# Performance work log

Measured on AMD Instinct MI355X. Metric: run time of the kernel, lower is better.

Reference implementation:

```python
import jax, jax.numpy as jnp
import numpy as np

N, E, F, S, R, H = 10000, 160000, 128, 10, 8, 64
SH_OFF = [0, 1, 4, 9]
SH_DIM = [1, 3, 5, 7]
AVG_NUM_NEIGHBORS = 16.0


def setup_inputs() -> dict:
    key = jax.random.key(0)
    ks = jax.random.split(key, 16)
    species = jax.random.randint(ks[0], (N,), 0, S)
    node_attrs = jax.nn.one_hot(species, S, dtype=jnp.float32)
    node_feats = jax.random.normal(ks[1], (N, F), dtype=jnp.float32)
    edge_attrs = jax.random.normal(ks[2], (E, 16), dtype=jnp.float32)
    edge_feats = jax.random.normal(ks[3], (E, R), dtype=jnp.float32)
    edge_index = jax.random.randint(ks[4], (2, E), 0, N)
    # learned parameters
    W_skip_node = jax.random.normal(ks[5], (F, S, F), dtype=jnp.float32)
    W_up = jax.random.normal(ks[6], (F, F), dtype=jnp.float32)
    mlp_w1 = jax.random.normal(ks[7], (R, H), dtype=jnp.float32)
    mlp_w2 = jax.random.normal(ks[8], (H, H), dtype=jnp.float32)
    mlp_w3 = jax.random.normal(ks[9], (H, H), dtype=jnp.float32)
    mlp_w4 = jax.random.normal(ks[10], (H, 4 * F), dtype=jnp.float32)  # conv_tp.weight_numel = 512
    W_lin = jax.random.normal(ks[11], (4, F, F), dtype=jnp.float32)
    W_skip_msg = jax.random.normal(ks[12], (4, F, S, F), dtype=jnp.float32)
    W_out = jax.random.normal(ks[13], (F, F), dtype=jnp.float32)
    return dict(node_attrs=node_attrs, node_feats=node_feats, edge_attrs=edge_attrs,
                edge_feats=edge_feats, edge_index=edge_index, species=species,
                W_skip_node=W_skip_node, W_up=W_up, mlp_w1=mlp_w1, mlp_w2=mlp_w2,
                mlp_w3=mlp_w3, mlp_w4=mlp_w4, W_lin=W_lin, W_skip_msg=W_skip_msg,
                W_out=W_out)


def reference(node_attrs, node_feats, edge_attrs, edge_feats, edge_index, species,
              W_skip_node, W_up, mlp_w1, mlp_w2, mlp_w3, mlp_w4,
              W_lin, W_skip_msg, W_out):
    sender, receiver = edge_index[0], edge_index[1]
    num_nodes = node_feats.shape[0]
    num_edges = edge_attrs.shape[0]

    # skip_tp_node: FullyConnectedTensorProduct(128x0e, 10x0e -> 128x0e), fan_in = 128*10
    skip = jnp.einsum('nu,nv,uvw->nw', node_feats, node_attrs, W_skip_node) * (1.0 / np.sqrt(F * S))

    # linear_up: 128x0e -> 128x0e
    h = (node_feats @ W_up) * (1.0 / np.sqrt(F))

    # radial MLP (e3nn FullyConnectedNet: no bias, w/sqrt(fan_in), silu on hidden layers)
    t = edge_feats
    for W in (mlp_w1, mlp_w2, mlp_w3):
        t = jax.nn.silu((t @ W) * (1.0 / np.sqrt(W.shape[0])))
    tp_w = (t @ mlp_w4) * (1.0 / np.sqrt(H))  # [E, 512]

    # conv_tp (gather -> 0e x l -> l 'uvu' TP) fused with scatter_sum per l-block
    hs = h[sender]  # [E, 128]
    msgs = []
    for l in range(4):
        d = SH_DIM[l]
        w_l = tp_w[:, l * F:(l + 1) * F]                       # [E, 128]
        sh_l = edge_attrs[:, SH_OFF[l]:SH_OFF[l] + d]          # [E, d]
        mji = (hs * w_l)[:, :, None] * sh_l[:, None, :]        # [E, 128, d]
        m = jax.ops.segment_sum(mji.reshape(num_edges, F * d), receiver,
                                num_segments=num_nodes)
        msgs.append(m.reshape(num_nodes, F, d))

    inv_avg = 1.0 / np.sqrt(AVG_NUM_NEIGHBORS)
    # linear (per-l 128->128) / sqrt(avg_num_neighbors), then skip_tp_msg (x 10x0e attrs)
    blocks = []
    for l in range(4):
        x = jnp.einsum('num,uw->nwm', msgs[l], W_lin[l]) * (inv_avg / np.sqrt(F))
        x = jnp.einsum('num,nv,uvw->nwm', x, node_attrs, W_skip_msg[l]) * (1.0 / np.sqrt(F * S))
        blocks.append(x)

    # linear_out: target -> 128x0e keeps only the scalar (l=0) block
    message = (blocks[0][:, :, 0] @ W_out) * (1.0 / np.sqrt(F))  # [N, 128]
    return message, skip
```

## Files before the change

kernel.cpp:

```cpp
#include <hip/hip_runtime.h>
#include <math.h>

#define NFEAT 128
#define NSPEC 10

__global__ void k_hist(const int* __restrict__ species, int* __restrict__ counts, int N) {
    int i = blockIdx.x * blockDim.x + threadIdx.x;
    if (i < N) atomicAdd(&counts[species[i]], 1);
}

__global__ void k_build(const int* __restrict__ counts, int* __restrict__ cursor,
                        int4* __restrict__ table, int* __restrict__ nTiles) {
    if (threadIdx.x == 0 && blockIdx.x == 0) {
        int off = 0, nt = 0;
        for (int s = 0; s < NSPEC; s++) {
            cursor[s] = off;
            int c = counts[s];
            for (int b = 0; b < c; b += 64)
                table[nt++] = make_int4(s, off + b, min(64, c - b), 0);
            off += c;
        }
        nTiles[0] = nt;
    }
}

__global__ void k_scatter(const int* __restrict__ species, int* __restrict__ cursor,
                          int* __restrict__ sorted, int N) {
    int i = blockIdx.x * blockDim.x + threadIdx.x;
    if (i < N) {
        int p = atomicAdd(&cursor[species[i]], 1);
        sorted[p] = i;
    }
}

__global__ void k_ehist(const int* __restrict__ edge_index, int* __restrict__ ehist, int E) {
    int i = blockIdx.x * blockDim.x + threadIdx.x;
    if (i < E) atomicAdd(&ehist[edge_index[E + i]], 1);
}

__global__ void k_escan(const int* __restrict__ ehist, int* __restrict__ ecursor, int N) {
    __shared__ int ssum[256];
    const int t = threadIdx.x;
    const int chunk = (N + 255) / 256;
    const int lo = t * chunk;
    const int hi = min(lo + chunk, N);
    int local = 0;
    for (int i = lo; i < hi; i++) local += ehist[i];
    ssum[t] = local;
    __syncthreads();
    for (int off = 1; off < 256; off <<= 1) {
        int x = (t >= off) ? ssum[t - off] : 0;
        __syncthreads();
        ssum[t] += x;
        __syncthreads();
    }
    int run = ssum[t] - local;
    for (int i = lo; i < hi; i++) {
        ecursor[i] = run;
        run += ehist[i];
    }
}

__global__ void k_escatter(const int* __restrict__ edge_index, int* __restrict__ ecursor,
                           int* __restrict__ eorder, int E) {
    int i = blockIdx.x * blockDim.x + threadIdx.x;
    if (i < E) {
        int r = edge_index[E + i];
        int p = atomicAdd(&ecursor[r], 1);
        eorder[p] = i;
    }
}

template <int BC>
__global__ __launch_bounds__(256) void k_gemm(
    const float* __restrict__ A, int aStride,
    const float* __restrict__ B, int bStride, int bSpecStride,
    float* __restrict__ C, int cStride, int cChunkY,
    int M, float alpha,
    const int* __restrict__ sorted,
    const int4* __restrict__ table,
    const int* __restrict__ nTiles)
{
    __shared__ float At[128][64];
    __shared__ float Bs[128][BC];
    const int t = threadIdx.x;
    const int gy = blockIdx.y;

    int start, cnt, spec = 0;
    if (table) {
        if (blockIdx.x >= nTiles[0]) return;
        int4 te = table[blockIdx.x];
        spec = te.x; start = te.y; cnt = te.z;
    } else {
        start = blockIdx.x * 64;
        cnt = M - start;
        if (cnt <= 0) return;
        if (cnt > 64) cnt = 64;
    }

    {
        const float* Bp = B + (long)spec * bSpecStride + (long)gy * BC;
        constexpr int F4R = BC / 4;
        #pragma unroll
        for (int i = 0; i < (128 * F4R) / 256; i++) {
            int idx = t + 256 * i;
            int k = idx / F4R;
            int c = (idx % F4R) * 4;
            *(float4*)&Bs[k][c] = *(const float4*)(Bp + (long)k * bStride + c);
        }
    }
    {
        int r = t & 63;
        int kc = (t >> 6) * 32;
        if (r < cnt) {
            int grow = table ? sorted[start + r] : (start + r);
            const float4* src = (const float4*)(A + (long)grow * aStride + kc);
            #pragma unroll
            for (int i = 0; i < 8; i++) {
                float4 v = src[i];
                At[kc + 4*i + 0][r] = v.x;
                At[kc + 4*i + 1][r] = v.y;
                At[kc + 4*i + 2][r] = v.z;
                At[kc + 4*i + 3][r] = v.w;
            }
        } else {
            #pragma unroll
            for (int i = 0; i < 32; i++) At[kc + i][r] = 0.0f;
        }
    }
    __syncthreads();

    constexpr int CG   = BC / 4;
    constexpr int ROWS = BC / 16;
    const int c0 = (t % CG) * 4;
    const int r0 = (t / CG) * ROWS;
    float acc[ROWS][4] = {};
    #pragma unroll 8
    for (int k = 0; k < 128; k++) {
        float4 b = *(const float4*)&Bs[k][c0];
        float av[ROWS];
        #pragma unroll
        for (int i = 0; i < ROWS / 4; i++) {
            float4 a = *(const float4*)&At[k][r0 + 4 * i];
            av[4*i + 0] = a.x; av[4*i + 1] = a.y; av[4*i + 2] = a.z; av[4*i + 3] = a.w;
        }
        #pragma unroll
        for (int i = 0; i < ROWS; i++) {
            acc[i][0] += av[i] * b.x;
            acc[i][1] += av[i] * b.y;
            acc[i][2] += av[i] * b.z;
            acc[i][3] += av[i] * b.w;
        }
    }
    #pragma unroll
    for (int i = 0; i < ROWS; i++) {
        int r = r0 + i;
        if (r < cnt) {
            int grow = table ? sorted[start + r] : (start + r);
            float4 v = make_float4(acc[i][0] * alpha, acc[i][1] * alpha,
                                   acc[i][2] * alpha, acc[i][3] * alpha);
            *(float4*)&C[(long)gy * cChunkY + (long)grow * cStride + c0] = v;
        }
    }
}

__global__ __launch_bounds__(256) void k_edge(
    const float* __restrict__ edge_attrs,
    const float* __restrict__ edge_feats,
    const int*   __restrict__ edge_index,
    const int*   __restrict__ eorder,
    const float* __restrict__ W1,
    const float* __restrict__ W2,
    const float* __restrict__ W3,
    const float* __restrict__ W4,
    const float* __restrict__ h,
    float*       __restrict__ msgs0,
    int E)
{
    __shared__ float W1s[8][64];
    __shared__ float W2s[64][64];
    __shared__ float W3s[64][64];
    __shared__ float efT[8][64];
    __shared__ float taT[64][64];
    __shared__ float tbT[64][64];
    __shared__ int   sendS[64];
    __shared__ int   recvS[64];
    __shared__ float sh0S[64];

    const int t = threadIdx.x;
    if (t < 128) ((float4*)W1s)[t] = ((const float4*)W1)[t];
    #pragma unroll
    for (int i = 0; i < 4; i++) {
        ((float4*)W2s)[t + 256 * i] = ((const float4*)W2)[t + 256 * i];
        ((float4*)W3s)[t + 256 * i] = ((const float4*)W3)[t + 256 * i];
    }
    __syncthreads();

    const float s1 = 0.3535533905932738f;
    const float s2 = 0.125f;

    const int e0 = (t & 15) * 4;
    const int j0 = (t >> 4) * 4;

    int ntiles = (E + 63) >> 6;
    for (int tile = blockIdx.x; tile < ntiles; tile += gridDim.x) {
        int ebase = tile << 6;
        if (t < 64) {
            int p = ebase + t;
            if (p < E) {
                int e = eorder[p];
                sendS[t] = edge_index[e];
                recvS[t] = edge_index[E + e];
                sh0S[t]  = edge_attrs[(long)e * 16];
            } else { sendS[t] = 0; recvS[t] = -1; sh0S[t] = 0.0f; }
        } else if (t < 128) {
            int l = t - 64;
            int p = ebase + l;
            if (p < E) {
                int e = eorder[p];
                const float4* src = (const float4*)(edge_feats + (long)e * 8);
                float4 v0 = src[0], v1 = src[1];
                efT[0][l] = v0.x; efT[1][l] = v0.y; efT[2][l] = v0.z; efT[3][l] = v0.w;
                efT[4][l] = v1.x; efT[5][l] = v1.y; efT[6][l] = v1.z; efT[7][l] = v1.w;
            } else {
                #pragma unroll
                for (int k = 0; k < 8; k++) efT[k][l] = 0.0f;
            }
        }
        __syncthreads();

        {
            float acc[4][4] = {};
            #pragma unroll
            for (int k = 0; k < 8; k++) {
                float4 a = *(const float4*)&efT[k][e0];
                float4 b = *(const float4*)&W1s[k][j0];
                float av[4] = {a.x, a.y, a.z, a.w};
                float bv[4] = {b.x, b.y, b.z, b.w};
                #pragma unroll
                for (int jj = 0; jj < 4; jj++)
                    #pragma unroll
                    for (int ee = 0; ee < 4; ee++)
                        acc[jj][ee] += av[ee] * bv[jj];
            }
            #pragma unroll
            for (int jj = 0; jj < 4; jj++) {
                float4 v; float x;
                x = acc[jj][0] * s1; v.x = x / (1.0f + expf(-x));
                x = acc[jj][1] * s1; v.y = x / (1.0f + expf(-x));
                x = acc[jj][2] * s1; v.z = x / (1.0f + expf(-x));
                x = acc[jj][3] * s1; v.w = x / (1.0f + expf(-x));
                *(float4*)&taT[j0 + jj][e0] = v;
            }
        }
        __syncthreads();

        {
            float acc[4][4] = {};
            #pragma unroll 4
            for (int k = 0; k < 64; k++) {
                float4 a = *(const float4*)&taT[k][e0];
                float4 b = *(const float4*)&W2s[k][j0];
                float av[4] = {a.x, a.y, a.z, a.w};
                float bv[4] = {b.x, b.y, b.z, b.w};
                #pragma unroll
                for (int jj = 0; jj < 4; jj++)
                    #pragma unroll
                    for (int ee = 0; ee < 4; ee++)
                        acc[jj][ee] += av[ee] * bv[jj];
            }
            #pragma unroll
            for (int jj = 0; jj < 4; jj++) {
                float4 v; float x;
                x = acc[jj][0] * s2; v.x = x / (1.0f + expf(-x));
                x = acc[jj][1] * s2; v.y = x / (1.0f + expf(-x));
                x = acc[jj][2] * s2; v.z = x / (1.0f + expf(-x));
                x = acc[jj][3] * s2; v.w = x / (1.0f + expf(-x));
                *(float4*)&tbT[j0 + jj][e0] = v;
            }
        }
        __syncthreads();

        {
            float acc[4][4] = {};
            #pragma unroll 4
            for (int k = 0; k < 64; k++) {
                float4 a = *(const float4*)&tbT[k][e0];
                float4 b = *(const float4*)&W3s[k][j0];
                float av[4] = {a.x, a.y, a.z, a.w};
                float bv[4] = {b.x, b.y, b.z, b.w};
                #pragma unroll
                for (int jj = 0; jj < 4; jj++)
                    #pragma unroll
                    for (int ee = 0; ee < 4; ee++)
                        acc[jj][ee] += av[ee] * bv[jj];
            }
            #pragma unroll
            for (int jj = 0; jj < 4; jj++) {
                float4 v; float x;
                x = acc[jj][0] * s2; v.x = x / (1.0f + expf(-x));
                x = acc[jj][1] * s2; v.y = x / (1.0f + expf(-x));
                x = acc[jj][2] * s2; v.z = x / (1.0f + expf(-x));
                x = acc[jj][3] * s2; v.w = x / (1.0f + expf(-x));
                *(float4*)&taT[j0 + jj][e0] = v;
            }
        }
        __syncthreads();

        {
            const int c0  = (t & 31) * 4;
            const int ew0 = (t >> 5) * 8;
            float acc[8][4] = {};
            #pragma unroll 4
            for (int k = 0; k < 64; k++) {
                float4 b  = *(const float4*)&W4[k * 512 + c0];
                float4 a0 = *(const float4*)&taT[k][ew0];
                float4 a1 = *(const float4*)&taT[k][ew0 + 4];
                float av[8] = {a0.x, a0.y, a0.z, a0.w, a1.x, a1.y, a1.z, a1.w};
                #pragma unroll
                for (int i = 0; i < 8; i++) {
                    acc[i][0] += av[i] * b.x;
                    acc[i][1] += av[i] * b.y;
                    acc[i][2] += av[i] * b.z;
                    acc[i][3] += av[i] * b.w;
                }
            }
            float4 sum = make_float4(0.f, 0.f, 0.f, 0.f);
            int cur = recvS[ew0];
            #pragma unroll
            for (int i = 0; i < 8; i++) {
                int el = ew0 + i;
                int rcv = recvS[el];
                float f = sh0S[el] * s2;
                int snd = sendS[el];
                float4 hv = *(const float4*)&h[(long)snd * NFEAT + c0];
                float4 v = make_float4(acc[i][0] * f * hv.x, acc[i][1] * f * hv.y,
                                       acc[i][2] * f * hv.z, acc[i][3] * f * hv.w);
                if (rcv != cur) {
                    if (cur >= 0) {
                        float* dst = msgs0 + (long)cur * NFEAT + c0;
                        atomicAdd(dst + 0, sum.x); atomicAdd(dst + 1, sum.y);
                        atomicAdd(dst + 2, sum.z); atomicAdd(dst + 3, sum.w);
                    }
                    cur = rcv; sum = v;
                } else {
                    sum.x += v.x; sum.y += v.y; sum.z += v.z; sum.w += v.w;
                }
            }
            if (cur >= 0) {
                float* dst = msgs0 + (long)cur * NFEAT + c0;
                atomicAdd(dst + 0, sum.x); atomicAdd(dst + 1, sum.y);
                atomicAdd(dst + 2, sum.z); atomicAdd(dst + 3, sum.w);
            }
        }
        __syncthreads();
    }
}

extern "C" void kernel_launch(void* const* d_in, const int* in_sizes, int n_in,
                              void* d_out, int out_size, void* d_ws, size_t ws_size,
                              hipStream_t stream) {
    const float* node_feats = (const float*)d_in[1];
    const float* edge_attrs = (const float*)d_in[2];
    const float* edge_feats = (const float*)d_in[3];
    const int*   edge_index = (const int*)  d_in[4];
    const int*   species    = (const int*)  d_in[5];
    const float* Wsn        = (const float*)d_in[6];
    const float* Wup        = (const float*)d_in[7];
    const float* W1         = (const float*)d_in[8];
    const float* W2         = (const float*)d_in[9];
    const float* W3         = (const float*)d_in[10];
    const float* W4         = (const float*)d_in[11];
    const float* Wlin       = (const float*)d_in[12];
    const float* Wsm        = (const float*)d_in[13];
    const float* Wout       = (const float*)d_in[14];

    const int N = in_sizes[5];
    const int E = in_sizes[4] / 2;
    const int NF = NFEAT;

    float* out     = (float*)d_out;
    float* message = out;
    float* skip    = out + (long)N * NF;

    char* wsb = (char*)d_ws;
    size_t off = 0;
    auto carve = [&](size_t bytes) { void* p = wsb + off; off = (off + bytes + 255) & ~(size_t)255; return p; };
    float* h      = (float*)carve((size_t)N * NF * 4);
    float* msgs0  = (float*)carve((size_t)N * NF * 4);
    float* Tst    = (float*)carve((size_t)NSPEC * NF * NF * 4);
    float* Comb   = (float*)carve((size_t)NSPEC * NF * NF * 4);
    int*   sorted = (int*)carve((size_t)N * 4);
    int*   counts = (int*)carve(64);
    int*   cursor = (int*)carve(64);
    int*   nTiles = (int*)carve(16);
    int4*  table  = (int4*)carve(256 * 16);
    int*   ehist  = (int*)carve((size_t)N * 4);
    int*   ecursor= (int*)carve((size_t)N * 4);
    int*   eorder = (int*)carve((size_t)E * 4);

    const float aH    = 1.0f / sqrtf((float)NF);
    const float aSkip = 1.0f / sqrtf((float)(NF * NSPEC));
    const float cTot  = 0.25f / ((float)NF * sqrtf((float)(NF * NSPEC)));

    hipMemsetAsync(counts, 0, 64, stream);
    hipMemsetAsync(ehist, 0, (size_t)N * 4, stream);
    hipMemsetAsync(msgs0, 0, (size_t)N * NF * 4, stream);

    k_hist   <<<(N + 255) / 256, 256, 0, stream>>>(species, counts, N);
    k_build  <<<1, 64, 0, stream>>>(counts, cursor, table, nTiles);
    k_scatter<<<(N + 255) / 256, 256, 0, stream>>>(species, cursor, sorted, N);

    k_ehist   <<<(E + 255) / 256, 256, 0, stream>>>(edge_index, ehist, E);
    k_escan   <<<1, 256, 0, stream>>>(ehist, ecursor, N);
    k_escatter<<<(E + 255) / 256, 256, 0, stream>>>(edge_index, ecursor, eorder, E);

    const int mTiles   = (N + 63) / 64;
    const int maxTiles = mTiles + NSPEC;

    k_gemm<64><<<dim3(mTiles, 2), 256, 0, stream>>>(
        node_feats, NF, Wup, NF, 0, h, NF, 64, N, aH, nullptr, nullptr, nullptr);

    k_gemm<128><<<dim3(2, NSPEC), 256, 0, stream>>>(
        Wlin, NF, Wsm, NF * NSPEC, 0, Tst, NF, NF * NF, NF, 1.0f, nullptr, nullptr, nullptr);

    k_gemm<128><<<dim3((NSPEC * NF) / 64, 1), 256, 0, stream>>>(
        Tst, NF, Wout, NF, 0, Comb, NF, NF, NSPEC * NF, cTot, nullptr, nullptr, nullptr);

    k_gemm<64><<<dim3(maxTiles, 2), 256, 0, stream>>>(
        node_feats, NF, Wsn, NF * NSPEC, NF, skip, NF, 64, N, aSkip, sorted, table, nTiles);

    int edgeTiles = (E + 63) / 64;
    int edgeGrid  = edgeTiles < 512 ? edgeTiles : 512;
    k_edge<<<edgeGrid, 256, 0, stream>>>(
        edge_attrs, edge_feats, edge_index, eorder, W1, W2, W3, W4, h, msgs0, E);

    k_gemm<64><<<dim3(maxTiles, 2), 256, 0, stream>>>(
        msgs0, NF, Comb, NF, NF * NF, message, NF, 64, N, 1.0f, sorted, table, nTiles);
}
```

Baseline: 397.6 us.

## Fuse histograms, pre-gather sorted edge data, shrink edge-kernel LDS, parallelize tile build

Merges the species and receiver histograms into one launch and parallelizes the tile-table build across threads. The edge scatter now writes sender, receiver, sh0 and edge features directly in receiver-sorted order, so the edge kernel reads contiguous data instead of doing indirect gathers. Inside the edge kernel the three activation buffers and the W3 shared copy collapse into one reused buffer, with extra barriers and W3 read from global memory. This cuts LDS use to allow more resident blocks, and the grid cap is doubled. It also switches to fast __expf. The cost is extra global traffic for the gathered arrays, more barriers, and slightly less accurate exponentials.

Measured after the change: 363.9 us. -8.5%, faster.

```diff
diff --git a/kernel.cpp b/kernel.cpp
--- a/kernel.cpp
+++ b/kernel.cpp
@@ -4,23 +4,35 @@
 #define NFEAT 128
 #define NSPEC 10
 
-__global__ void k_hist(const int* __restrict__ species, int* __restrict__ counts, int N) {
+__global__ void k_histboth(const int* __restrict__ species, const int* __restrict__ edge_index,
+                           int* __restrict__ counts, int* __restrict__ ehist, int N, int E) {
     int i = blockIdx.x * blockDim.x + threadIdx.x;
     if (i < N) atomicAdd(&counts[species[i]], 1);
+    if (i < E) atomicAdd(&ehist[edge_index[E + i]], 1);
 }
 
 __global__ void k_build(const int* __restrict__ counts, int* __restrict__ cursor,
                         int4* __restrict__ table, int* __restrict__ nTiles) {
-    if (threadIdx.x == 0 && blockIdx.x == 0) {
-        int off = 0, nt = 0;
+    __shared__ int off[NSPEC + 1], ts[NSPEC + 1], cnt[NSPEC];
+    const int t = threadIdx.x;
+    if (t == 0) {
+        int o = 0, tt = 0;
         for (int s = 0; s < NSPEC; s++) {
-            cursor[s] = off;
-            int c = counts[s];
-            for (int b = 0; b < c; b += 64)
-                table[nt++] = make_int4(s, off + b, min(64, c - b), 0);
-            off += c;
-        }
-        nTiles[0] = nt;
+            cnt[s] = counts[s];
+            off[s] = o; ts[s] = tt;
+            o += cnt[s]; tt += (cnt[s] + 63) >> 6;
+        }
+        off[NSPEC] = o; ts[NSPEC] = tt;
+        nTiles[0] = tt;
+    }
+    __syncthreads();
+    if (t < NSPEC) cursor[t] = off[t];
+    int nt = ts[NSPEC];
+    for (int i = t; i < nt; i += blockDim.x) {
+        int s = 0;
+        while (ts[s + 1] <= i) s++;
+        int b = i - ts[s];
+        table[i] = make_int4(s, off[s] + b * 64, min(64, cnt[s] - b * 64), 0);
     }
 }
 
@@ -31,11 +43,6 @@
         int p = atomicAdd(&cursor[species[i]], 1);
         sorted[p] = i;
     }
-}
-
-__global__ void k_ehist(const int* __restrict__ edge_index, int* __restrict__ ehist, int E) {
-    int i = blockIdx.x * blockDim.x + threadIdx.x;
-    if (i < E) atomicAdd(&ehist[edge_index[E + i]], 1);
 }
 
 __global__ void k_escan(const int* __restrict__ ehist, int* __restrict__ ecursor, int N) {
@@ -61,13 +68,21 @@
     }
 }
 
-__global__ void k_escatter(const int* __restrict__ edge_index, int* __restrict__ ecursor,
-                           int* __restrict__ eorder, int E) {
+__global__ void k_egather(const int* __restrict__ edge_index, const float* __restrict__ edge_attrs,
+                          const float* __restrict__ edge_feats, int* __restrict__ ecursor,
+                          int* __restrict__ sendG, int* __restrict__ recvG,
+                          float* __restrict__ sh0G, float* __restrict__ efG, int E) {
     int i = blockIdx.x * blockDim.x + threadIdx.x;
     if (i < E) {
         int r = edge_index[E + i];
         int p = atomicAdd(&ecursor[r], 1);
-        eorder[p] = i;
+        sendG[p] = edge_index[i];
+        recvG[p] = r;
+        sh0G[p]  = edge_attrs[(long)i * 16];
+        float4 v0 = *(const float4*)(edge_feats + (long)i * 8);
+        float4 v1 = *(const float4*)(edge_feats + (long)i * 8 + 4);
+        *(float4*)(efG + (long)p * 8)     = v0;
+        *(float4*)(efG + (long)p * 8 + 4) = v1;
     }
 }
 
@@ -165,10 +180,10 @@
 }
 
 __global__ __launch_bounds__(256) void k_edge(
-    const float* __restrict__ edge_attrs,
-    const float* __restrict__ edge_feats,
-    const int*   __restrict__ edge_index,
-    const int*   __restrict__ eorder,
+    const int*   __restrict__ sendG,
+    const int*   __restrict__ recvG,
+    const float* __restrict__ sh0G,
+    const float* __restrict__ efG,
     const float* __restrict__ W1,
     const float* __restrict__ W2,
     const float* __restrict__ W3,
@@ -179,10 +194,8 @@
 {
     __shared__ float W1s[8][64];
     __shared__ float W2s[64][64];
-    __shared__ float W3s[64][64];
+    __shared__ float act[64][64];
     __shared__ float efT[8][64];
-    __shared__ float taT[64][64];
-    __shared__ float tbT[64][64];
     __shared__ int   sendS[64];
     __shared__ int   recvS[64];
     __shared__ float sh0S[64];
@@ -190,10 +203,8 @@
     const int t = threadIdx.x;
     if (t < 128) ((float4*)W1s)[t] = ((const float4*)W1)[t];
     #pragma unroll
-    for (int i = 0; i < 4; i++) {
+    for (int i = 0; i < 4; i++)
         ((float4*)W2s)[t + 256 * i] = ((const float4*)W2)[t + 256 * i];
-        ((float4*)W3s)[t + 256 * i] = ((const float4*)W3)[t + 256 * i];
-    }
     __syncthreads();
 
     const float s1 = 0.3535533905932738f;
@@ -208,18 +219,16 @@
         if (t < 64) {
             int p = ebase + t;
             if (p < E) {
-                int e = eorder[p];
-                sendS[t] = edge_index[e];
-                recvS[t] = edge_index[E + e];
-                sh0S[t]  = edge_attrs[(long)e * 16];
+                sendS[t] = sendG[p];
+                recvS[t] = recvG[p];
+                sh0S[t]  = sh0G[p];
             } else { sendS[t] = 0; recvS[t] = -1; sh0S[t] = 0.0f; }
         } else if (t < 128) {
             int l = t - 64;
             int p = ebase + l;
             if (p < E) {
-                int e = eorder[p];
-                const float4* src = (const float4*)(edge_feats + (long)e * 8);
-                float4 v0 = src[0], v1 = src[1];
+                float4 v0 = *(const float4*)(efG + (long)p * 8);
+                float4 v1 = *(const float4*)(efG + (long)p * 8 + 4);
                 efT[0][l] = v0.x; efT[1][l] = v0.y; efT[2][l] = v0.z; efT[3][l] = v0.w;
                 efT[4][l] = v1.x; efT[5][l] = v1.y; efT[6][l] = v1.z; efT[7][l] = v1.w;
             } else {
@@ -246,11 +255,11 @@
             #pragma unroll
             for (int jj = 0; jj < 4; jj++) {
                 float4 v; float x;
-                x = acc[jj][0] * s1; v.x = x / (1.0f + expf(-x));
-                x = acc[jj][1] * s1; v.y = x / (1.0f + expf(-x));
-                x = acc[jj][2] * s1; v.z = x / (1.0f + expf(-x));
-                x = acc[jj][3] * s1; v.w = x / (1.0f + expf(-x));
-                *(float4*)&taT[j0 + jj][e0] = v;
+                x = acc[jj][0] * s1; v.x = x / (1.0f + __expf(-x));
+                x = acc[jj][1] * s1; v.y = x / (1.0f + __expf(-x));
+                x = acc[jj][2] * s1; v.z = x / (1.0f + __expf(-x));
+                x = acc[jj][3] * s1; v.w = x / (1.0f + __expf(-x));
+                *(float4*)&act[j0 + jj][e0] = v;
             }
         }
         __syncthreads();
@@ -259,7 +268,7 @@
             float acc[4][4] = {};
             #pragma unroll 4
             for (int k = 0; k < 64; k++) {
-                float4 a = *(const float4*)&taT[k][e0];
+                float4 a = *(const float4*)&act[k][e0];
                 float4 b = *(const float4*)&W2s[k][j0];
                 float av[4] = {a.x, a.y, a.z, a.w};
                 float bv[4] = {b.x, b.y, b.z, b.w};
@@ -269,14 +278,15 @@
                     for (int ee = 0; ee < 4; ee++)
                         acc[jj][ee] += av[ee] * bv[jj];
             }
+            __syncthreads();
             #pragma unroll
             for (int jj = 0; jj < 4; jj++) {
                 float4 v; float x;
-                x = acc[jj][0] * s2; v.x = x / (1.0f + expf(-x));
-                x = acc[jj][1] * s2; v.y = x / (1.0f + expf(-x));
-                x = acc[jj][2] * s2; v.z = x / (1.0f + expf(-x));
-                x = acc[jj][3] * s2; v.w = x / (1.0f + expf(-x));
-                *(float4*)&tbT[j0 + jj][e0] = v;
+                x = acc[jj][0] * s2; v.x = x / (1.0f + __expf(-x));
+                x = acc[jj][1] * s2; v.y = x / (1.0f + __expf(-x));
+                x = acc[jj][2] * s2; v.z = x / (1.0f + __expf(-x));
+                x = acc[jj][3] * s2; v.w = x / (1.0f + __expf(-x));
+                *(float4*)&act[j0 + jj][e0] = v;
             }
         }
         __syncthreads();
@@ -285,8 +295,8 @@
             float acc[4][4] = {};
             #pragma unroll 4
             for (int k = 0; k < 64; k++) {
-                float4 a = *(const float4*)&tbT[k][e0];
-                float4 b = *(const float4*)&W3s[k][j0];
+                float4 a = *(const float4*)&act[k][e0];
+                float4 b = *(const float4*)(W3 + k * 64 + j0);
                 float av[4] = {a.x, a.y, a.z, a.w};
                 float bv[4] = {b.x, b.y, b.z, b.w};
                 #pragma unroll
@@ -295,14 +305,15 @@
                     for (int ee = 0; ee < 4; ee++)
                         acc[jj][ee] += av[ee] * bv[jj];
             }
+            __syncthreads();
             #pragma unroll
             for (int jj = 0; jj < 4; jj++) {
                 float4 v; float x;
-                x = acc[jj][0] * s2; v.x = x / (1.0f + expf(-x));
-                x = acc[jj][1] * s2; v.y = x / (1.0f + expf(-x));
-                x = acc[jj][2] * s2; v.z = x / (1.0f + expf(-x));
-                x = acc[jj][3] * s2; v.w = x / (1.0f + expf(-x));
-                *(float4*)&taT[j0 + jj][e0] = v;
+                x = acc[jj][0] * s2; v.x = x / (1.0f + __expf(-x));
+                x = acc[jj][1] * s2; v.y = x / (1.0f + __expf(-x));
+                x = acc[jj][2] * s2; v.z = x / (1.0f + __expf(-x));
+                x = acc[jj][3] * s2; v.w = x / (1.0f + __expf(-x));
+                *(float4*)&act[j0 + jj][e0] = v;
             }
         }
         __syncthreads();
@@ -314,8 +325,8 @@
             #pragma unroll 4
             for (int k = 0; k < 64; k++) {
                 float4 b  = *(const float4*)&W4[k * 512 + c0];
-                float4 a0 = *(const float4*)&taT[k][ew0];
-                float4 a1 = *(const float4*)&taT[k][ew0 + 4];
+                float4 a0 = *(const float4*)&act[k][ew0];
+                float4 a1 = *(const float4*)&act[k][ew0 + 4];
                 float av[8] = {a0.x, a0.y, a0.z, a0.w, a1.x, a1.y, a1.z, a1.w};
                 #pragma unroll
                 for (int i = 0; i < 8; i++) {
@@ -397,7 +408,10 @@
     int4*  table  = (int4*)carve(256 * 16);
     int*   ehist  = (int*)carve((size_t)N * 4);
     int*   ecursor= (int*)carve((size_t)N * 4);
-    int*   eorder = (int*)carve((size_t)E * 4);
+    int*   sendG  = (int*)carve((size_t)E * 4);
+    int*   recvG  = (int*)carve((size_t)E * 4);
+    float* sh0G   = (float*)carve((size_t)E * 4);
+    float* efG    = (float*)carve((size_t)E * 8 * 4);
 
     const float aH    = 1.0f / sqrtf((float)NF);
     const float aSkip = 1.0f / sqrtf((float)(NF * NSPEC));
@@ -407,13 +421,12 @@
     hipMemsetAsync(ehist, 0, (size_t)N * 4, stream);
     hipMemsetAsync(msgs0, 0, (size_t)N * NF * 4, stream);
 
-    k_hist   <<<(N + 255) / 256, 256, 0, stream>>>(species, counts, N);
-    k_build  <<<1, 64, 0, stream>>>(counts, cursor, table, nTiles);
+    k_histboth<<<(max(N, E) + 255) / 256, 256, 0, stream>>>(species, edge_index, counts, ehist, N, E);
+    k_build  <<<1, 256, 0, stream>>>(counts, cursor, table, nTiles);
     k_scatter<<<(N + 255) / 256, 256, 0, stream>>>(species, cursor, sorted, N);
-
-    k_ehist   <<<(E + 255) / 256, 256, 0, stream>>>(edge_index, ehist, E);
-    k_escan   <<<1, 256, 0, stream>>>(ehist, ecursor, N);
-    k_escatter<<<(E + 255) / 256, 256, 0, stream>>>(edge_index, ecursor, eorder, E);
+    k_escan  <<<1, 256, 0, stream>>>(ehist, ecursor, N);
+    k_egather<<<(E + 255) / 256, 256, 0, stream>>>(edge_index, edge_attrs, edge_feats,
+                                                   ecursor, sendG, recvG, sh0G, efG, E);
 
     const int mTiles   = (N + 63) / 64;
     const int maxTiles = mTiles + NSPEC;
@@ -431,9 +444,9 @@
         node_feats, NF, Wsn, NF * NSPEC, NF, skip, NF, 64, N, aSkip, sorted, table, nTiles);
 
     int edgeTiles = (E + 63) / 64;
-    int edgeGrid  = edgeTiles < 512 ? edgeTiles : 512;
+    int edgeGrid  = edgeTiles < 1024 ? edgeTiles : 1024;
     k_edge<<<edgeGrid, 256, 0, stream>>>(
-        edge_attrs, edge_feats, edge_index, eorder, W1, W2, W3, W4, h, msgs0, E);
+        sendG, recvG, sh0G, efG, W1, W2, W3, W4, h, msgs0, E);
 
     k_gemm<64><<<dim3(maxTiles, 2), 256, 0, stream>>>(
         msgs0, NF, Comb, NF, NF * NF, message, NF, 64, N, 1.0f, sorted, table, nTiles);
```
